# Kernel tuning notes

Hardware: AMD Instinct MI355X
Metric: run time of the kernel (lower is better)

The kernel has to match this reference:

```python
import jax, jax.numpy as jnp
import numpy as np

N_NODES = 100000
D_FEAT = 128
N_EDGES = 1000000


def setup_inputs() -> dict:
    key = jax.random.key(0)
    k_h, k_a, k_b = jax.random.split(key, 3)
    h = jax.random.normal(k_h, (N_NODES, D_FEAT), dtype=jnp.float32)
    edges_a = jax.random.randint(k_a, (2, N_EDGES), 0, N_NODES, dtype=jnp.int64)
    edges_b = jax.random.randint(k_b, (2, N_EDGES), 0, N_NODES, dtype=jnp.int64)
    return {"h": h, "edges_a": edges_a, "edges_b": edges_b}


def _u_dot_v(h, edges):
    # gather src/dst node embeddings, per-edge dot product -> [E]
    src, dst = edges[0], edges[1]
    return jnp.sum(h[src] * h[dst], axis=-1)


def reference(h, edges_a, edges_b):
    # EdgePredictor with loss_type='CONTRASTIVE': sigmoid(u . v) per etype
    score_a = jax.nn.sigmoid(_u_dot_v(h, edges_a))
    score_b = jax.nn.sigmoid(_u_dot_v(h, edges_b))
    return (score_a, score_b)
```

## Files before the change

kernel.cpp:

```cpp
#include <hip/hip_runtime.h>
#include <hip/hip_fp16.h>


#define N_NODES 100000
#define D_FEAT  128
#define N_EDGES 1000000
#define NTOT    (2 * N_EDGES)
#define NB      32
#define BLOCK_ROWS ((N_NODES + NB - 1) / NB)
#define CAP     65536
#define NSLOTS  (NB * CAP)

#define CURSOR_OFF 256
#define H16_OFF    4096
#define H16_BYTES  ((size_t)N_NODES * D_FEAT * 2)
#define PACKED_OFF (H16_OFF + H16_BYTES)
#define PACKED_BYTES ((size_t)NSLOTS * 8)
#define WS_NEED    (PACKED_OFF + PACKED_BYTES)

#define CONV_BLOCKS (N_NODES * D_FEAT / 8 / 256)
#define SORT_GRID   ((NTOT + 2047) / 2048)
#define PRE_GROUPS  123
#define PRE_GRID    (PRE_GROUPS * 64)

typedef float f4v __attribute__((ext_vector_type(4)));

__device__ __forceinline__ int detect64(const void* ea) {
    const long long* p = (const long long*)ea;
    int is64 = 1;
    #pragma unroll
    for (int i = 0; i < 8; ++i) {
        long long v = p[i];
        if (v < 0 || v >= N_NODES) is64 = 0;
    }
    return is64;
}

__device__ __forceinline__ void load_edge(const void* ea, const void* eb,
                                          int is64, long long e,
                                          int& s, int& d) {
    if (e < N_EDGES) {
        if (is64) {
            s = (int)((const long long*)ea)[e];
            d = (int)((const long long*)ea)[e + N_EDGES];
        } else {
            s = ((const int*)ea)[e];
            d = ((const int*)ea)[e + N_EDGES];
        }
    } else {
        long long e2 = e - N_EDGES;
        if (is64) {
            s = (int)((const long long*)eb)[e2];
            d = (int)((const long long*)eb)[e2 + N_EDGES];
        } else {
            s = ((const int*)eb)[e2];
            d = ((const int*)eb)[e2 + N_EDGES];
        }
    }
}

__global__ __launch_bounds__(256) void pre_kernel(
    const float* __restrict__ h, __half* __restrict__ hh,
    const void* __restrict__ ea, const void* __restrict__ eb,
    int* __restrict__ cursor, unsigned long long* __restrict__ packed) {
    int bid = blockIdx.x;
    int tid = threadIdx.x;
    int grp = bid >> 6;
    int sub = bid & 63;
    if (sub >= 8) {
        int cidx = grp * 56 + sub - 8;
        if (cidx >= CONV_BLOCKS) return;
        int i = cidx * 256 + tid;
        const float4* src = (const float4*)h;
        float4 a = src[2 * i];
        float4 b = src[2 * i + 1];
        __half2 r[4];
        r[0] = __float22half2_rn(make_float2(a.x, a.y));
        r[1] = __float22half2_rn(make_float2(a.z, a.w));
        r[2] = __float22half2_rn(make_float2(b.x, b.y));
        r[3] = __float22half2_rn(make_float2(b.z, b.w));
        ((float4*)hh)[i] = *(const float4*)r;
        return;
    }
    int sidx = grp * 8 + sub;
    if (sidx >= SORT_GRID) return;
    __shared__ int lh[NB];
    __shared__ int lcur[NB];
    if (tid < NB) lh[tid] = 0;
    __syncthreads();
    const int is64 = detect64(ea);
    long long base = (long long)sidx * 2048;
    int ss[8], dd[8], ee[8];
    int cnt = 0;
    #pragma unroll
    for (int i = 0; i < 8; ++i) {
        long long e = base + i * 256 + tid;
        if (e >= NTOT) break;
        int s, d;
        load_edge(ea, eb, is64, e, s, d);
        ss[cnt] = s; dd[cnt] = d; ee[cnt] = (int)e; ++cnt;
        atomicAdd(&lh[s / BLOCK_ROWS], 1);
    }
    __syncthreads();
    if (tid < NB)
        lcur[tid] = tid * CAP + atomicAdd(&cursor[tid], lh[tid]);
    __syncthreads();
    for (int i = 0; i < cnt; ++i) {
        int b = ss[i] / BLOCK_ROWS;
        int pos = atomicAdd(&lcur[b], 1);
        packed[pos] = (unsigned long long)ss[i]
                    | ((unsigned long long)dd[i] << 17)
                    | ((unsigned long long)ee[i] << 34);
    }
}

#define MAIN_GRID (NSLOTS / 64)
#define GRID_PER_XCD (MAIN_GRID / 8)

__device__ __forceinline__ float dot8_f16(f4v sv, f4v dv, float acc) {
    const __half2* s2 = (const __half2*)&sv;
    const __half2* d2 = (const __half2*)&dv;
#if __has_builtin(__builtin_amdgcn_fdot2)
    #pragma unroll
    for (int j = 0; j < 4; ++j)
        acc = __builtin_amdgcn_fdot2(s2[j], d2[j], acc, false);
#else
    #pragma unroll
    for (int j = 0; j < 4; ++j) {
        float2 sf = __half22float2(s2[j]);
        float2 df = __half22float2(d2[j]);
        acc += sf.x * df.x + sf.y * df.y;
    }
#endif
    return acc;
}

__global__ __launch_bounds__(256) void edge_main_sorted(
    const __half* __restrict__ hh,
    const unsigned long long* __restrict__ packed,
    const int* __restrict__ cnt,
    float* __restrict__ out) {
    int bid = blockIdx.x;
    int swz = (bid & 7) * GRID_PER_XCD + (bid >> 3);
    int gid = swz * 256 + threadIdx.x;
    int grp  = gid >> 3;
    int lane = gid & 7;
    int slot0 = grp << 1;
    int b = slot0 >> 16;
    int cb = cnt[b];
    int l0 = slot0 & (CAP - 1);
    if (l0 >= cb) return;
    bool v1 = (l0 + 1) < cb;

    ulonglong2 pp = *(const ulonglong2*)(packed + slot0);
    unsigned long long p0 = pp.x;
    unsigned long long p1 = v1 ? pp.y : pp.x;
    int s0 = (int)(p0 & 0x1FFFF), d0 = (int)((p0 >> 17) & 0x1FFFF), e0 = (int)(p0 >> 34);
    int s1 = (int)(p1 & 0x1FFFF), d1 = (int)((p1 >> 17) & 0x1FFFF), e1 = (int)(p1 >> 34);

    const f4v* ps0 = (const f4v*)(hh + (size_t)s0 * D_FEAT) + lane * 2;
    const f4v* pd0 = (const f4v*)(hh + (size_t)d0 * D_FEAT) + lane * 2;
    const f4v* ps1 = (const f4v*)(hh + (size_t)s1 * D_FEAT) + lane * 2;
    const f4v* pd1 = (const f4v*)(hh + (size_t)d1 * D_FEAT) + lane * 2;
    f4v sa0 = ps0[0], sb0 = ps0[1];
    f4v da0 = pd0[0], db0 = pd0[1];
    f4v sa1 = ps1[0], sb1 = ps1[1];
    f4v da1 = pd1[0], db1 = pd1[1];

    float acc0 = dot8_f16(sb0, db0, dot8_f16(sa0, da0, 0.0f));
    float acc1 = dot8_f16(sb1, db1, dot8_f16(sa1, da1, 0.0f));
    acc0 += __shfl_xor(acc0, 4, 64);
    acc0 += __shfl_xor(acc0, 2, 64);
    acc0 += __shfl_xor(acc0, 1, 64);
    acc1 += __shfl_xor(acc1, 4, 64);
    acc1 += __shfl_xor(acc1, 2, 64);
    acc1 += __shfl_xor(acc1, 1, 64);

    if (lane == 0) {
        out[e0] = 1.0f / (1.0f + expf(-acc0));
        if (v1) out[e1] = 1.0f / (1.0f + expf(-acc1));
    }
}

__global__ __launch_bounds__(256) void convert_h_fp16(
    const float* __restrict__ h, __half* __restrict__ hh) {
    int i = blockIdx.x * 256 + threadIdx.x;
    if (i >= N_NODES * D_FEAT / 8) return;
    const float4* src = (const float4*)h;
    float4 a = src[2 * i];
    float4 b = src[2 * i + 1];
    __half2 r[4];
    r[0] = __float22half2_rn(make_float2(a.x, a.y));
    r[1] = __float22half2_rn(make_float2(a.z, a.w));
    r[2] = __float22half2_rn(make_float2(b.x, b.y));
    r[3] = __float22half2_rn(make_float2(b.z, b.w));
    ((float4*)hh)[i] = *(const float4*)r;
}

__global__ __launch_bounds__(256) void edge_pred_fp16(
    const __half* __restrict__ hh,
    const void* __restrict__ ea, const void* __restrict__ eb,
    float* __restrict__ out) {
    int gid  = blockIdx.x * 256 + threadIdx.x;
    int edge = gid >> 3;
    int lane = gid & 7;
    if (edge >= NTOT) return;
    const int is64 = detect64(ea);
    int s, d;
    load_edge(ea, eb, is64, (long long)edge, s, d);
    const f4v* ps = (const f4v*)(hh + (size_t)s * D_FEAT) + lane * 2;
    const f4v* pd = (const f4v*)(hh + (size_t)d * D_FEAT) + lane * 2;
    f4v s0 = ps[0], s1 = ps[1], d0 = pd[0], d1 = pd[1];
    float acc = dot8_f16(s1, d1, dot8_f16(s0, d0, 0.0f));
    acc += __shfl_xor(acc, 4, 64);
    acc += __shfl_xor(acc, 2, 64);
    acc += __shfl_xor(acc, 1, 64);
    if (lane == 0)
        out[edge] = 1.0f / (1.0f + expf(-acc));
}

__global__ __launch_bounds__(256) void edge_pred_fp32(
    const float* __restrict__ h,
    const void* __restrict__ ea, const void* __restrict__ eb,
    float* __restrict__ out) {
    int gid  = blockIdx.x * 256 + threadIdx.x;
    int edge = gid >> 4;
    int lane = gid & 15;
    if (edge >= NTOT) return;
    const int is64 = detect64(ea);
    int s, d;
    load_edge(ea, eb, is64, (long long)edge, s, d);
    const float4* ps = (const float4*)(h + (size_t)s * D_FEAT) + lane * 2;
    const float4* pd = (const float4*)(h + (size_t)d * D_FEAT) + lane * 2;
    float4 s0 = ps[0], s1 = ps[1], d0 = pd[0], d1 = pd[1];
    float acc = s0.x * d0.x + s0.y * d0.y + s0.z * d0.z + s0.w * d0.w
              + s1.x * d1.x + s1.y * d1.y + s1.z * d1.z + s1.w * d1.w;
    #pragma unroll
    for (int off = 8; off >= 1; off >>= 1)
        acc += __shfl_xor(acc, off, 64);
    if (lane == 0)
        out[edge] = 1.0f / (1.0f + expf(-acc));
}

extern "C" void kernel_launch(void* const* d_in, const int* in_sizes, int n_in,
                              void* d_out, int out_size, void* d_ws, size_t ws_size,
                              hipStream_t stream) {
    const float* h  = (const float*)d_in[0];
    const void*  ea = d_in[1];
    const void*  eb = d_in[2];
    float* out = (float*)d_out;
    char* ws = (char*)d_ws;

    const int block = 256;

    if (ws_size >= WS_NEED) {
        __half* hh  = (__half*)(ws + H16_OFF);
        int* cursor = (int*)(ws + CURSOR_OFF);
        unsigned long long* packed = (unsigned long long*)(ws + PACKED_OFF);

        hipMemsetAsync(cursor, 0, NB * sizeof(int), stream);
        pre_kernel<<<PRE_GRID, block, 0, stream>>>(h, hh, ea, eb, cursor, packed);
        edge_main_sorted<<<MAIN_GRID, block, 0, stream>>>(hh, packed, cursor, out);
    } else if (ws_size >= H16_OFF + H16_BYTES) {
        __half* hh = (__half*)(ws + H16_OFF);
        convert_h_fp16<<<CONV_BLOCKS, block, 0, stream>>>(h, hh);
        const long long tt = (long long)NTOT * 8;
        edge_pred_fp16<<<(int)((tt + block - 1) / block), block, 0, stream>>>(hh, ea, eb, out);
    } else {
        const long long tt = (long long)NTOT * 16;
        edge_pred_fp32<<<(int)((tt + block - 1) / block), block, 0, stream>>>(h, ea, eb, out);
    }
}
```

Before: 127.1 us.

## Fuse preprocessing and edge scoring into one cooperative kernel with grid sync

Replaces the two-kernel sequence (scatter/convert pre-kernel, then sorted edge scoring) with a single cooperative kernel of 2048 persistent blocks. Some blocks bucket the edges while the rest convert h to fp16 in a grid-stride loop, then a grid-wide barrier separates this phase from the scoring phase, which loops over 16 virtual blocks per real block. The aim is to remove one kernel launch and the gap between kernels. In exchange it adds grid-sync cost, fewer resident threads for the gather phase, and host-side occupancy and attribute queries on every call, with a fallback to the old path.

```diff
diff --git a/kernel.cpp b/kernel.cpp
--- a/kernel.cpp
+++ b/kernel.cpp
@@ -1,5 +1,8 @@
 #include <hip/hip_runtime.h>
 #include <hip/hip_fp16.h>
+#include <hip/hip_cooperative_groups.h>
+
+namespace cg = cooperative_groups;
 
 
 #define N_NODES 100000
@@ -18,10 +21,10 @@
 #define PACKED_BYTES ((size_t)NSLOTS * 8)
 #define WS_NEED    (PACKED_OFF + PACKED_BYTES)
 
-#define CONV_BLOCKS (N_NODES * D_FEAT / 8 / 256)
+#define CONV_ITEMS  (N_NODES * D_FEAT / 8)
+#define CONV_BLOCKS (CONV_ITEMS / 256)
 #define SORT_GRID   ((NTOT + 2047) / 2048)
-#define PRE_GROUPS  123
-#define PRE_GRID    (PRE_GROUPS * 64)
+#define COOP_BLOCKS 2048
 
 typedef float f4v __attribute__((ext_vector_type(4)));
 
@@ -59,33 +62,41 @@
     }
 }
 
-__global__ __launch_bounds__(256) void pre_kernel(
-    const float* __restrict__ h, __half* __restrict__ hh,
-    const void* __restrict__ ea, const void* __restrict__ eb,
-    int* __restrict__ cursor, unsigned long long* __restrict__ packed) {
-    int bid = blockIdx.x;
-    int tid = threadIdx.x;
-    int grp = bid >> 6;
-    int sub = bid & 63;
-    if (sub >= 8) {
-        int cidx = grp * 56 + sub - 8;
-        if (cidx >= CONV_BLOCKS) return;
-        int i = cidx * 256 + tid;
-        const float4* src = (const float4*)h;
-        float4 a = src[2 * i];
-        float4 b = src[2 * i + 1];
-        __half2 r[4];
-        r[0] = __float22half2_rn(make_float2(a.x, a.y));
-        r[1] = __float22half2_rn(make_float2(a.z, a.w));
-        r[2] = __float22half2_rn(make_float2(b.x, b.y));
-        r[3] = __float22half2_rn(make_float2(b.z, b.w));
-        ((float4*)hh)[i] = *(const float4*)r;
-        return;
-    }
-    int sidx = grp * 8 + sub;
-    if (sidx >= SORT_GRID) return;
-    __shared__ int lh[NB];
-    __shared__ int lcur[NB];
+__device__ __forceinline__ void convert8(const float* __restrict__ h,
+                                         __half* __restrict__ hh, int i) {
+    const float4* src = (const float4*)h;
+    float4 a = src[2 * i];
+    float4 b = src[2 * i + 1];
+    __half2 r[4];
+    r[0] = __float22half2_rn(make_float2(a.x, a.y));
+    r[1] = __float22half2_rn(make_float2(a.z, a.w));
+    r[2] = __float22half2_rn(make_float2(b.x, b.y));
+    r[3] = __float22half2_rn(make_float2(b.z, b.w));
+    ((float4*)hh)[i] = *(const float4*)r;
+}
+
+__device__ __forceinline__ float dot8_f16(f4v sv, f4v dv, float acc) {
+    const __half2* s2 = (const __half2*)&sv;
+    const __half2* d2 = (const __half2*)&dv;
+#if __has_builtin(__builtin_amdgcn_fdot2)
+    #pragma unroll
+    for (int j = 0; j < 4; ++j)
+        acc = __builtin_amdgcn_fdot2(s2[j], d2[j], acc, false);
+#else
+    #pragma unroll
+    for (int j = 0; j < 4; ++j) {
+        float2 sf = __half22float2(s2[j]);
+        float2 df = __half22float2(d2[j]);
+        acc += sf.x * df.x + sf.y * df.y;
+    }
+#endif
+    return acc;
+}
+
+__device__ __forceinline__ void scatter_chunk(
+    const void* ea, const void* eb, int sidx,
+    int* cursor, unsigned long long* packed,
+    int* lh, int* lcur, int tid) {
     if (tid < NB) lh[tid] = 0;
     __syncthreads();
     const int is64 = detect64(ea);
@@ -114,26 +125,100 @@
     }
 }
 
+__device__ __forceinline__ void main_pair(
+    const __half* __restrict__ hh,
+    const unsigned long long* __restrict__ packed,
+    float* __restrict__ out, int slot0, int cb, int lane) {
+    int l0 = slot0 & (CAP - 1);
+    if (l0 >= cb) return;
+    bool v1 = (l0 + 1) < cb;
+    ulonglong2 pp = *(const ulonglong2*)(packed + slot0);
+    unsigned long long p0 = pp.x;
+    unsigned long long p1 = v1 ? pp.y : pp.x;
+    int s0 = (int)(p0 & 0x1FFFF), d0 = (int)((p0 >> 17) & 0x1FFFF), e0 = (int)(p0 >> 34);
+    int s1 = (int)(p1 & 0x1FFFF), d1 = (int)((p1 >> 17) & 0x1FFFF), e1 = (int)(p1 >> 34);
+
+    const f4v* ps0 = (const f4v*)(hh + (size_t)s0 * D_FEAT) + lane * 2;
+    const f4v* pd0 = (const f4v*)(hh + (size_t)d0 * D_FEAT) + lane * 2;
+    const f4v* ps1 = (const f4v*)(hh + (size_t)s1 * D_FEAT) + lane * 2;
+    const f4v* pd1 = (const f4v*)(hh + (size_t)d1 * D_FEAT) + lane * 2;
+    f4v sa0 = ps0[0], sb0 = ps0[1];
+    f4v da0 = pd0[0], db0 = pd0[1];
+    f4v sa1 = ps1[0], sb1 = ps1[1];
+    f4v da1 = pd1[0], db1 = pd1[1];
+
+    float acc0 = dot8_f16(sb0, db0, dot8_f16(sa0, da0, 0.0f));
+    float acc1 = dot8_f16(sb1, db1, dot8_f16(sa1, da1, 0.0f));
+    acc0 += __shfl_xor(acc0, 4, 64);
+    acc0 += __shfl_xor(acc0, 2, 64);
+    acc0 += __shfl_xor(acc0, 1, 64);
+    acc1 += __shfl_xor(acc1, 4, 64);
+    acc1 += __shfl_xor(acc1, 2, 64);
+    acc1 += __shfl_xor(acc1, 1, 64);
+
+    if (lane == 0) {
+        out[e0] = 1.0f / (1.0f + expf(-acc0));
+        if (v1) out[e1] = 1.0f / (1.0f + expf(-acc1));
+    }
+}
+
+__global__ __launch_bounds__(256, 8) void fused_all(
+    const float* __restrict__ h, __half* __restrict__ hh,
+    const void* __restrict__ ea, const void* __restrict__ eb,
+    int* __restrict__ cursor, unsigned long long* __restrict__ packed,
+    float* __restrict__ out) {
+    __shared__ int lh[NB];
+    __shared__ int lcur[NB];
+    int bid = blockIdx.x;
+    int tid = threadIdx.x;
+
+    if (bid < SORT_GRID) {
+        scatter_chunk(ea, eb, bid, cursor, packed, lh, lcur, tid);
+    } else {
+        const int stride = (COOP_BLOCKS - SORT_GRID) * 256;
+        for (int i = (bid - SORT_GRID) * 256 + tid; i < CONV_ITEMS; i += stride)
+            convert8(h, hh, i);
+    }
+
+    cg::this_grid().sync();
+
+    int x = bid & 7;
+    int inner = bid >> 3;
+    int g = tid >> 3, lane = tid & 7;
+    #pragma unroll 1
+    for (int t = 0; t < 16; ++t) {
+        int vb = x * 4096 + t * 256 + inner;
+        int slot0 = vb * 64 + g * 2;
+        int b = slot0 >> 16;
+        main_pair(hh, packed, out, slot0, cursor[b], lane);
+    }
+}
+
+__global__ __launch_bounds__(256) void pre_kernel(
+    const float* __restrict__ h, __half* __restrict__ hh,
+    const void* __restrict__ ea, const void* __restrict__ eb,
+    int* __restrict__ cursor, unsigned long long* __restrict__ packed) {
+    __shared__ int lh[NB];
+    __shared__ int lcur[NB];
+    int bid = blockIdx.x;
+    int tid = threadIdx.x;
+    int grp = bid >> 6;
+    int sub = bid & 63;
+    if (sub >= 8) {
+        int cidx = grp * 56 + sub - 8;
+        if (cidx >= CONV_BLOCKS) return;
+        convert8(h, hh, cidx * 256 + tid);
+        return;
+    }
+    int sidx = grp * 8 + sub;
+    if (sidx >= SORT_GRID) return;
+    scatter_chunk(ea, eb, sidx, cursor, packed, lh, lcur, tid);
+}
+
+#define PRE_GROUPS 123
+#define PRE_GRID   (PRE_GROUPS * 64)
 #define MAIN_GRID (NSLOTS / 64)
 #define GRID_PER_XCD (MAIN_GRID / 8)
-
-__device__ __forceinline__ float dot8_f16(f4v sv, f4v dv, float acc) {
-    const __half2* s2 = (const __half2*)&sv;
-    const __half2* d2 = (const __half2*)&dv;
-#if __has_builtin(__builtin_amdgcn_fdot2)
-    #pragma unroll
-    for (int j = 0; j < 4; ++j)
-        acc = __builtin_amdgcn_fdot2(s2[j], d2[j], acc, false);
-#else
-    #pragma unroll
-    for (int j = 0; j < 4; ++j) {
-        float2 sf = __half22float2(s2[j]);
-        float2 df = __half22float2(d2[j]);
-        acc += sf.x * df.x + sf.y * df.y;
-    }
-#endif
-    return acc;
-}
 
 __global__ __launch_bounds__(256) void edge_main_sorted(
     const __half* __restrict__ hh,
@@ -147,54 +232,14 @@
     int lane = gid & 7;
     int slot0 = grp << 1;
     int b = slot0 >> 16;
-    int cb = cnt[b];
-    int l0 = slot0 & (CAP - 1);
-    if (l0 >= cb) return;
-    bool v1 = (l0 + 1) < cb;
-
-    ulonglong2 pp = *(const ulonglong2*)(packed + slot0);
-    unsigned long long p0 = pp.x;
-    unsigned long long p1 = v1 ? pp.y : pp.x;
-    int s0 = (int)(p0 & 0x1FFFF), d0 = (int)((p0 >> 17) & 0x1FFFF), e0 = (int)(p0 >> 34);
-    int s1 = (int)(p1 & 0x1FFFF), d1 = (int)((p1 >> 17) & 0x1FFFF), e1 = (int)(p1 >> 34);
-
-    const f4v* ps0 = (const f4v*)(hh + (size_t)s0 * D_FEAT) + lane * 2;
-    const f4v* pd0 = (const f4v*)(hh + (size_t)d0 * D_FEAT) + lane * 2;
-    const f4v* ps1 = (const f4v*)(hh + (size_t)s1 * D_FEAT) + lane * 2;
-    const f4v* pd1 = (const f4v*)(hh + (size_t)d1 * D_FEAT) + lane * 2;
-    f4v sa0 = ps0[0], sb0 = ps0[1];
-    f4v da0 = pd0[0], db0 = pd0[1];
-    f4v sa1 = ps1[0], sb1 = ps1[1];
-    f4v da1 = pd1[0], db1 = pd1[1];
-
-    float acc0 = dot8_f16(sb0, db0, dot8_f16(sa0, da0, 0.0f));
-    float acc1 = dot8_f16(sb1, db1, dot8_f16(sa1, da1, 0.0f));
-    acc0 += __shfl_xor(acc0, 4, 64);
-    acc0 += __shfl_xor(acc0, 2, 64);
-    acc0 += __shfl_xor(acc0, 1, 64);
-    acc1 += __shfl_xor(acc1, 4, 64);
-    acc1 += __shfl_xor(acc1, 2, 64);
-    acc1 += __shfl_xor(acc1, 1, 64);
-
-    if (lane == 0) {
-        out[e0] = 1.0f / (1.0f + expf(-acc0));
-        if (v1) out[e1] = 1.0f / (1.0f + expf(-acc1));
-    }
+    main_pair(hh, packed, out, slot0, cnt[b], lane);
 }
 
 __global__ __launch_bounds__(256) void convert_h_fp16(
     const float* __restrict__ h, __half* __restrict__ hh) {
     int i = blockIdx.x * 256 + threadIdx.x;
-    if (i >= N_NODES * D_FEAT / 8) return;
-    const float4* src = (const float4*)h;
-    float4 a = src[2 * i];
-    float4 b = src[2 * i + 1];
-    __half2 r[4];
-    r[0] = __float22half2_rn(make_float2(a.x, a.y));
-    r[1] = __float22half2_rn(make_float2(a.z, a.w));
-    r[2] = __float22half2_rn(make_float2(b.x, b.y));
-    r[3] = __float22half2_rn(make_float2(b.z, b.w));
-    ((float4*)hh)[i] = *(const float4*)r;
+    if (i >= CONV_ITEMS) return;
+    convert8(h, hh, i);
 }
 
 __global__ __launch_bounds__(256) void edge_pred_fp16(
@@ -259,8 +304,27 @@
         unsigned long long* packed = (unsigned long long*)(ws + PACKED_OFF);
 
         hipMemsetAsync(cursor, 0, NB * sizeof(int), stream);
-        pre_kernel<<<PRE_GRID, block, 0, stream>>>(h, hh, ea, eb, cursor, packed);
-        edge_main_sorted<<<MAIN_GRID, block, 0, stream>>>(hh, packed, cursor, out);
+
+        int dev = 0;
+        hipGetDevice(&dev);
+        int coop = 0, cus = 0, perCU = 0;
+        hipDeviceGetAttribute(&coop, hipDeviceAttributeCooperativeLaunch, dev);
+        hipDeviceGetAttribute(&cus, hipDeviceAttributeMultiprocessorCount, dev);
+        hipOccupancyMaxActiveBlocksPerMultiprocessor(&perCU, fused_all, block, 0);
+
+        bool launched = false;
+        if (coop && (long long)cus * perCU >= COOP_BLOCKS) {
+            void* args[] = {(void*)&h, (void*)&hh, (void*)&ea, (void*)&eb,
+                            (void*)&cursor, (void*)&packed, (void*)&out};
+            hipError_t err = hipLaunchCooperativeKernel(
+                (const void*)fused_all, dim3(COOP_BLOCKS), dim3(block),
+                args, 0, stream);
+            launched = (err == hipSuccess);
+        }
+        if (!launched) {
+            pre_kernel<<<PRE_GRID, block, 0, stream>>>(h, hh, ea, eb, cursor, packed);
+            edge_main_sorted<<<MAIN_GRID, block, 0, stream>>>(hh, packed, cursor, out);
+        }
     } else if (ws_size >= H16_OFF + H16_BYTES) {
         __half* hh = (__half*)(ws + H16_OFF);
         convert_h_fp16<<<CONV_BLOCKS, block, 0, stream>>>(h, hh);
```

After: 127.8 us. Within noise of the previous version (+0.5%).
